# Performance work log

Hardware: AMD Instinct MI355X
Metric: run time of the kernel (lower is better)

Reference implementation:

```python
import jax, jax.numpy as jnp
import numpy as np

DIM, HEADS, DH, M, PINV_ITERS, RES_K = 512, 8, 64, 256, 6, 33

def layernorm(x, w, b, eps=1e-5):
    mu = jnp.mean(x, -1, keepdims=True)
    var = jnp.var(x, -1, keepdims=True)
    return (x - mu) * jax.lax.rsqrt(var + eps) * w + b

def pinv_iter(x, iters=PINV_ITERS):
    # Moore-Penrose iterative pseudo-inverse (lucidrains nystrom-attention)
    ax = jnp.abs(x)
    z = jnp.swapaxes(x, -1, -2) / (jnp.max(ax.sum(-1)) * jnp.max(ax.sum(-2)))
    I = jnp.eye(x.shape[-1], dtype=x.dtype)
    for _ in range(iters):
        xz = x @ z
        z = 0.25 * z @ (13 * I - xz @ (15 * I - xz @ (7 * I - xz)))
    return z

def _core(x, w_qkv):
    b, n, _ = x.shape
    pad = (M - n % M) % M            # Nystrom pads at the FRONT to a multiple of m=256
    xp = jnp.pad(x, ((0, 0), (pad, 0), (0, 0)))
    npad = n + pad
    q, k, v = jnp.split(xp @ w_qkv, 3, axis=-1)
    split_heads = lambda t: t.reshape(b, npad, HEADS, DH).transpose(0, 2, 1, 3)
    q = split_heads(q) * (DH ** -0.5)
    k, v = split_heads(k), split_heads(v)
    l = npad // M                    # tokens per landmark
    q_l = q.reshape(b, HEADS, M, l, DH).mean(3)
    k_l = k.reshape(b, HEADS, M, l, DH).mean(3)
    return q, k, v, q_l, k_l, pad, n

def nystrom_out(x, w_qkv, w_out, b_out, res_kernel):
    q, k, v, q_l, k_l, pad, n = _core(x, w_qkv)
    attn1 = jax.nn.softmax(jnp.einsum('bhid,bhjd->bhij', q, k_l), -1)    # (b,h,N,M)
    attn2 = jax.nn.softmax(jnp.einsum('bhid,bhjd->bhij', q_l, k_l), -1)  # (b,h,M,M)
    attn3 = jax.nn.softmax(jnp.einsum('bhid,bhjd->bhij', q_l, k), -1)    # (b,h,M,N)
    out = (attn1 @ pinv_iter(attn2)) @ (attn3 @ v)
    # depthwise residual conv over sequence dim, per head
    out = out + jax.lax.conv_general_dilated(
        v, res_kernel, (1, 1), [(RES_K // 2, RES_K // 2), (0, 0)],
        dimension_numbers=('NCHW', 'OIHW', 'NCHW'), feature_group_count=HEADS)
    b = out.shape[0]
    out = out.transpose(0, 2, 1, 3).reshape(b, -1, HEADS * DH) @ w_out + b_out
    return out[:, -n:]

def nystrom_cls_row(x, w_qkv):
    # cls-token (query index pad, head 0) row of attn1 @ pinv(attn2) @ attn3;
    # identical math to the full (n x n) matrix row the torch code slices out.
    q, k, v, q_l, k_l, pad, n = _core(x, w_qkv)
    q0, k0, ql0, kl0 = q[:, 0], k[:, 0], q_l[:, 0], k_l[:, 0]
    attn2 = jax.nn.softmax(ql0 @ jnp.swapaxes(kl0, -1, -2), -1)   # (b,M,M)
    attn3 = jax.nn.softmax(ql0 @ jnp.swapaxes(k0, -1, -2), -1)    # (b,M,N)
    row1 = jax.nn.softmax(jnp.einsum('bd,bjd->bj', q0[:, pad], kl0), -1)
    row = jnp.einsum('bj,bjk->bk', row1, pinv_iter(attn2))
    row = jnp.einsum('bk,bkn->bn', row, attn3)                    # (b, N_padded)
    return row, pad

def dwconv(x, k, b, p):
    y = jax.lax.conv_general_dilated(x, k, (1, 1), [(p, p), (p, p)],
        dimension_numbers=('NCHW', 'OIHW', 'NCHW'), feature_group_count=x.shape[1])
    return y + b[None, :, None, None]

def leff(x, k7, b7, k5, b5, k3, b3, Hs, Ws):
    cls_t, feat = x[:, :1], x[:, 1:]
    B, N, C = feat.shape
    img = feat.transpose(0, 2, 1).reshape(B, C, Hs, Ws)
    y = dwconv(img, k7, b7, 3) + img + dwconv(img, k5, b5, 2) + dwconv(img, k3, b3, 1)
    y = y.reshape(B, C, Hs * Ws).transpose(0, 2, 1)
    return jnp.concatenate([cls_t, y], axis=1)

def setup_inputs():
    key = jax.random.key(0)
    ks = iter(jax.random.split(key, 32))
    n, n_classes = 22500, 2
    p = {}
    p['h'] = jax.random.normal(next(ks), (n, 1024), jnp.float32)
    p['fc1_w'] = jax.random.normal(next(ks), (1024, DIM), jnp.float32) * 0.02
    p['fc1_b'] = jnp.zeros((DIM,), jnp.float32)
    p['cls_token'] = jax.random.normal(next(ks), (1, 1, DIM), jnp.float32)
    for pre in ('l1', 'l2'):
        p[pre + '_ln_w'] = jnp.ones((DIM,), jnp.float32)
        p[pre + '_ln_b'] = jnp.zeros((DIM,), jnp.float32)
        p[pre + '_wqkv'] = jax.random.normal(next(ks), (DIM, 3 * HEADS * DH), jnp.float32) * 0.02
        p[pre + '_wout'] = jax.random.normal(next(ks), (HEADS * DH, DIM), jnp.float32) * 0.02
        p[pre + '_bout'] = jnp.zeros((DIM,), jnp.float32)
        p[pre + '_resk'] = jax.random.normal(next(ks), (HEADS, 1, RES_K, 1), jnp.float32) * 0.05
    for kk in (7, 5, 3):
        p['leff_k%d' % kk] = jax.random.normal(next(ks), (DIM, 1, kk, kk), jnp.float32) * 0.05
        p['leff_b%d' % kk] = jnp.zeros((DIM,), jnp.float32)
    p['norm_w'] = jnp.ones((DIM,), jnp.float32)
    p['norm_b'] = jnp.zeros((DIM,), jnp.float32)
    p['fc2_w'] = jax.random.normal(next(ks), (DIM, n_classes), jnp.float32) * 0.02
    p['fc2_b'] = jnp.zeros((n_classes,), jnp.float32)
    return p

def reference(h, fc1_w, fc1_b, cls_token,
              l1_ln_w, l1_ln_b, l1_wqkv, l1_wout, l1_bout, l1_resk,
              leff_k7, leff_b7, leff_k5, leff_b5, leff_k3, leff_b3,
              l2_ln_w, l2_ln_b, l2_wqkv, l2_wout, l2_bout, l2_resk,
              norm_w, norm_b, fc2_w, fc2_b):
    x = h[None]                                   # (1, n, 1024)
    n = x.shape[1]
    x = jax.nn.relu(x @ fc1_w + fc1_b)            # (1, n, 512)
    Hs = int(np.ceil(np.sqrt(n)))                 # 150 for n=22500
    add_len = Hs * Hs - n
    if add_len > 0:
        x = jnp.concatenate([x, x[:, :add_len]], axis=1)
    x = jnp.concatenate([jnp.broadcast_to(cls_token, (1, 1, DIM)), x], axis=1)
    # TransLayer 1
    x = x + nystrom_out(layernorm(x, l1_ln_w, l1_ln_b), l1_wqkv, l1_wout, l1_bout, l1_resk)
    # LeFF positional layer
    x = leff(x, leff_k7, leff_b7, leff_k5, leff_b5, leff_k3, leff_b3, Hs, Hs)
    # TransLayer 2 (first call in TransMIL.forward)
    h2 = x + nystrom_out(layernorm(x, l2_ln_w, l2_ln_b), l2_wqkv, l2_wout, l2_bout, l2_resk)
    # TransLayer 2 second call: residual update then attention matrix of updated state
    h3 = h2 + nystrom_out(layernorm(h2, l2_ln_w, l2_ln_b), l2_wqkv, l2_wout, l2_bout, l2_resk)
    row, pad = nystrom_cls_row(layernorm(h3, l2_ln_w, l2_ln_b), l2_wqkv)
    A = row[0, pad + 1: pad + 1 + n][:, None]     # (n, 1) cls->instance attention
    hf = layernorm(h2, norm_w, norm_b)[:, 0]      # (1, 512)
    logits = hf @ fc2_w + fc2_b                   # (1, n_classes)
    Y_prob = jax.nn.softmax(logits, -1)
    return logits, Y_prob, A
```

## Files before the change

kernel.cpp:

```cpp
#include <hip/hip_runtime.h>

#define NTOK 22500
#define N1   22501
#define NPAD 22528
#define PADR 27
#define DIM  512
#define NH   8
#define DHD  64
#define MM   256
#define LLM  88
#define HSZ  150
#define CSZ  256
#define NCH  88

typedef short bf16x8 __attribute__((ext_vector_type(8)));
typedef float f32x4  __attribute__((ext_vector_type(4)));
typedef unsigned short us;

union U8 { bf16x8 v; unsigned short u[8]; };

__device__ __forceinline__ unsigned short f2b(float f){
  unsigned int u = __float_as_uint(f);
  unsigned int r = u + 0x7fffu + ((u>>16)&1u);
  return (unsigned short)(r>>16);
}
__device__ __forceinline__ float bf2f(unsigned short u){
  return __uint_as_float(((unsigned int)u)<<16);
}
__device__ __forceinline__ bf16x8 cvt8(float4 a, float4 b){
  U8 u;
  u.u[0]=f2b(a.x); u.u[1]=f2b(a.y); u.u[2]=f2b(a.z); u.u[3]=f2b(a.w);
  u.u[4]=f2b(b.x); u.u[5]=f2b(b.y); u.u[6]=f2b(b.z); u.u[7]=f2b(b.w);
  return u.v;
}
__device__ __forceinline__ void gld16(const void* g, void* l){
  __builtin_amdgcn_global_load_lds(
      (const __attribute__((address_space(1))) void*)g,
      (__attribute__((address_space(3))) void*)l, 16, 0, 0);
}

__device__ __forceinline__ float waveSum(float v){
#pragma unroll
  for (int o=32;o>0;o>>=1) v += __shfl_down(v,o);
  return v;
}
__device__ __forceinline__ float waveMax(float v){
#pragma unroll
  for (int o=32;o>0;o>>=1) v = fmaxf(v,__shfl_down(v,o));
  return v;
}
__device__ __forceinline__ float blockSum256(float v, float* sb){
  v = waveSum(v);
  __syncthreads();
  if ((threadIdx.x&63)==0) sb[threadIdx.x>>6]=v;
  __syncthreads();
  return sb[0]+sb[1]+sb[2]+sb[3];
}
__device__ __forceinline__ float blockMax256(float v, float* sb){
  v = waveMax(v);
  __syncthreads();
  if ((threadIdx.x&63)==0) sb[threadIdx.x>>6]=v;
  __syncthreads();
  return fmaxf(fmaxf(sb[0],sb[1]),fmaxf(sb[2],sb[3]));
}

__global__ void k_wT(const float* __restrict__ W, us* __restrict__ Bt, int K, int N)
{
  __shared__ float tile[32][33];
  int tx = threadIdx.x&31, ty = threadIdx.x>>5;
  int k0 = blockIdx.x*32, n0 = blockIdx.y*32;
#pragma unroll
  for (int i=0;i<4;++i){
    int k = k0+ty+i*8;
    if (k<K && n0+tx<N) tile[ty+i*8][tx] = W[(size_t)k*N + n0+tx];
  }
  __syncthreads();
#pragma unroll
  for (int i=0;i<4;++i){
    int n = n0+ty+i*8, k = k0+tx;
    if (n<N && k<K) Bt[(size_t)n*K + k] = f2b(tile[tx][ty+i*8]);
  }
}

__global__ void k_vT(const us* __restrict__ V, us* __restrict__ Vt)
{
  __shared__ us tile[32][33];
  int tx = threadIdx.x&31, ty = threadIdx.x>>5;
  int p0 = blockIdx.x*32;
  int h = blockIdx.y>>1, d0 = (blockIdx.y&1)*32;
#pragma unroll
  for (int i=0;i<4;++i){
    int p = p0+ty+i*8;
    tile[ty+i*8][tx] = V[((size_t)h*NPAD+p)*DHD + d0+tx];
  }
  __syncthreads();
#pragma unroll
  for (int i=0;i<4;++i){
    int d = d0+ty+i*8;
    Vt[((size_t)h*DHD+d)*NPAD + p0+tx] = tile[tx][ty+i*8];
  }
}

template<int MODE, int BM>
__global__ __launch_bounds__(256) void k_gemm(const float* __restrict__ Af,
    const us* __restrict__ Ab, const us* __restrict__ Bt, const float* __restrict__ bias,
    us* __restrict__ Xb, float* __restrict__ Cf, float* __restrict__ C2,
    us* __restrict__ Q_, us* __restrict__ K_, us* __restrict__ V_,
    const us* __restrict__ zpg, int Kd, int mtn)
{
  constexpr int ABUF = BM*64;
  __shared__ us SM[2*ABUF + 16384];
  const int tid = threadIdx.x;
  const int bid = blockIdx.x;
  const int ntile = bid / mtn;
  const int m0 = (bid % mtn)*BM, n0 = ntile*128;
  const int lane = tid & 63;
  const int wid = tid >> 6;
  constexpr int MT = BM/32;
  constexpr int ACH = BM/32;
  const int wm = (wid>>1)*(BM/2), wn = (wid&1)*64;
  f32x4 acc[MT][4] = {};
  const int NT = Kd >> 6;

  auto stage = [&](int t, int buf){
    us* As = SM + buf*ABUF;
    us* Bs = SM + 2*ABUF + buf*8192;
    int k0 = t*64;
    if (MODE==0){
#pragma unroll
      for (int i=0;i<BM/16;++i){
        int g = i*256 + tid;
        int row = g>>4, k4 = (g&15)*4;
        int gm = m0 + row;
        ushort4 h4 = make_ushort4(0,0,0,0);
        if (gm < NTOK){
          float4 v = *(const float4*)(Af + (size_t)gm*Kd + k0 + k4);
          h4.x=f2b(v.x); h4.y=f2b(v.y); h4.z=f2b(v.z); h4.w=f2b(v.w);
        }
        *(ushort4*)(&As[row*64 + (k4 ^ ((row&7)<<3))]) = h4;
      }
    } else {
#pragma unroll
      for (int i=0;i<ACH;++i){
        int c = wid*ACH+i;
        int row = c*8 + (lane>>3);
        int scol8 = ((lane&7) ^ (row&7))*8;
        int gm = m0+row;
        const us* ga;
        if (MODE==2) ga = Ab + ((size_t)((gm<N1?gm:0)+PADR))*Kd + k0 + scol8;
        else ga = (gm>=PADR) ? Ab + (size_t)(gm-PADR)*Kd + k0 + scol8 : zpg + scol8;
        gld16(ga, &As[c*512]);
      }
    }
#pragma unroll
    for (int i=0;i<4;++i){
      int c = wid*4+i;
      int row = c*8 + (lane>>3);
      int scol8 = ((lane&7) ^ (row&7))*8;
      int vn = n0+row;
      if (MODE==3) vn = (vn<64)? vn : vn+448;
      gld16(Bt + (size_t)vn*Kd + k0 + scol8, &Bs[c*512]);
    }
  };

  stage(0, 0);
  __syncthreads();
  for (int t=0; t<NT; ++t){
    const int cur = t&1;
    if (t+1 < NT) stage(t+1, cur^1);
    us* As = SM + cur*ABUF;
    us* Bs = SM + 2*ABUF + cur*8192;
#pragma unroll
    for (int ks=0; ks<2; ++ks){
      const int kk = ks*32 + (lane>>4)*8;
      bf16x8 af[MT], bfm[4];
#pragma unroll
      for (int tt=0;tt<MT;++tt){
        int r = wm + tt*16 + (lane&15);
        af[tt] = *(bf16x8*)(&As[r*64 + (kk ^ ((r&7)<<3))]);
      }
#pragma unroll
      for (int tt=0;tt<4;++tt){
        int c = wn + tt*16 + (lane&15);
        bfm[tt] = *(bf16x8*)(&Bs[c*64 + (kk ^ ((c&7)<<3))]);
      }
#pragma unroll
      for (int mt=0;mt<MT;++mt)
#pragma unroll
        for (int nt=0;nt<4;++nt)
          acc[mt][nt] = __builtin_amdgcn_mfma_f32_16x16x32_bf16(af[mt], bfm[nt], acc[mt][nt], 0,0,0);
    }
    __syncthreads();
  }
  const int rbase = (lane>>4)*4;
  const int cl = lane&15;
  if (MODE==3){
#pragma unroll
    for (int mt=0;mt<MT;++mt)
#pragma unroll
      for (int r=0;r<4;++r){
        int gm = m0 + wm + mt*16 + rbase + r;
#pragma unroll
        for (int nt=0;nt<4;++nt){
          int gn = n0 + wn + nt*16 + cl;
          float v = acc[mt][nt][r];
          if (gn < 64) Cf[(size_t)gm*DHD + gn] = v*0.125f;
          else         C2[(size_t)gm*DHD + (gn-64)] = v;
        }
      }
    return;
  }
  const float sc1 = (MODE==1 && (ntile>>2)==0) ? 0.125f : 1.f;
#pragma unroll
  for (int mt=0;mt<MT;++mt)
#pragma unroll
    for (int r=0;r<4;++r){
      int row = wm + mt*16 + rbase + r;
#pragma unroll
      for (int nt=0;nt<4;++nt){
        int col = wn + nt*16 + cl;
        float v = acc[mt][nt][r];
        if (MODE==0){ v += bias[n0+col]; v = v>0.f?v:0.f; }
        else if (MODE==2){ v += bias[n0+col]; }
        else v *= sc1;
        SM[row*128 + col] = f2b(v);
      }
    }
  __syncthreads();
  if (MODE==1){
    const int sec = ntile>>2;
    us* dst = sec==0 ? Q_ : (sec==1 ? K_ : V_);
#pragma unroll
    for (int i=0;i<BM/16;++i){
      int v8 = i*256 + tid;
      int row = v8>>4, c8 = (v8&15)*8;
      int gm = m0 + row, gn = n0 + c8;
      int hh = (gn>>6)&7, d = gn&63;
      *(bf16x8*)(dst + ((size_t)hh*NPAD+gm)*DHD + d) = *(bf16x8*)(&SM[row*128 + c8]);
    }
  } else if (MODE==0){
#pragma unroll
    for (int i=0;i<BM/16;++i){
      int v8 = i*256 + tid;
      int row = v8>>4, c8 = (v8&15)*8;
      int gm = m0 + row;
      if (gm < NTOK)
        *(bf16x8*)(Xb + (size_t)(1+gm)*DIM + n0 + c8) = *(bf16x8*)(&SM[row*128 + c8]);
    }
  } else {
#pragma unroll
    for (int i=0;i<BM/16;++i){
      int v8 = i*256 + tid;
      int row = v8>>4, c8 = (v8&15)*8;
      int gm = m0 + row;
      if (gm < N1){
        us* p = Xb + (size_t)gm*DIM + n0 + c8;
        U8 xo, ad, o;
        xo.v = *(bf16x8*)p;
        ad.v = *(bf16x8*)(&SM[row*128 + c8]);
#pragma unroll
        for (int j=0;j<8;++j) o.u[j] = f2b(bf2f(xo.u[j]) + bf2f(ad.u[j]));
        *(bf16x8*)p = o.v;
      }
    }
  }
}

__global__ void k_setcls(us* __restrict__ X, const float* __restrict__ cls){
  int i = blockIdx.x*256 + threadIdx.x;
  if (i < DIM) X[i] = f2b(cls[i]);
}
__global__ void k_copyu(us* __restrict__ d, const us* __restrict__ s, size_t n){
  size_t i = (size_t)blockIdx.x*256 + threadIdx.x;
  if (i<n) d[i]=s[i];
}

__global__ void k_ln(const us* __restrict__ X, us* __restrict__ Y,
                     const float* __restrict__ w, const float* __restrict__ b)
{
  __shared__ float sb[4];
  const us* x = X + (size_t)blockIdx.x*DIM;
  us* y = Y + (size_t)blockIdx.x*DIM;
  int t = threadIdx.x;
  ushort2 xv = *(const ushort2*)(x + 2*t);
  float a0=bf2f(xv.x), a1=bf2f(xv.y);
  float s = blockSum256(a0+a1, sb);
  float q = blockSum256(a0*a0+a1*a1, sb);
  float mean = s*(1.f/512.f);
  float var = q*(1.f/512.f) - mean*mean;
  float rstd = rsqrtf(var+1e-5f);
  float2 wv = *(const float2*)(w + 2*t);
  float2 bv = *(const float2*)(b + 2*t);
  ushort2 o;
  o.x = f2b((a0-mean)*rstd*wv.x+bv.x);
  o.y = f2b((a1-mean)*rstd*wv.y+bv.y);
  *(ushort2*)(y + 2*t) = o;
}

__global__ void k_landmark2(const us* __restrict__ Q, const us* __restrict__ K,
                            us* __restrict__ QL, us* __restrict__ KL)
{
  int hm = blockIdx.x;
  bool isK = hm >= NH*MM;
  if (isK) hm -= NH*MM;
  int h = hm>>8, m = hm&255; int d = threadIdx.x;
  const us* base = (isK?K:Q) + ((size_t)h*NPAD + (size_t)m*LLM)*DHD + d;
  float s = 0.f;
  for (int j=0;j<LLM;++j) s += bf2f(base[(size_t)j*DHD]);
  (isK?KL:QL)[((size_t)h*MM + m)*DHD + d] = f2b(s * (1.f/(float)LLM));
}
__global__ void k_landmark2f(const float* __restrict__ Q, const float* __restrict__ K,
                             float* __restrict__ QL, float* __restrict__ KL)
{
  int hm = blockIdx.x;
  bool isK = hm >= MM;
  int m = isK ? hm-MM : hm; int d = threadIdx.x;
  const float* base = (isK?K:Q) + (size_t)m*LLM*DHD + d;
  float s = 0.f;
  for (int j=0;j<LLM;++j) s += base[(size_t)j*DHD];
  (isK?KL:QL)[(size_t)m*DHD + d] = s * (1.f/(float)LLM);
}

__global__ __launch_bounds__(64) void k_nt64(const float* __restrict__ A,
    const float* __restrict__ B, float* __restrict__ C,
    long sA, long sB, long sC, int Nr)
{
  int lane = threadIdx.x;
  int n0 = blockIdx.x*64, m0 = blockIdx.y*64;
  A += (size_t)blockIdx.z*sA; B += (size_t)blockIdx.z*sB; C += (size_t)blockIdx.z*sC;
  f32x4 acc[4][4] = {};
#pragma unroll
  for (int ks=0;ks<2;++ks){
    int kk = ks*32 + (lane>>4)*8;
    bf16x8 af[4], bfr[4];
#pragma unroll
    for (int mt=0;mt<4;++mt){
      const float* p = A + (size_t)(m0+mt*16+(lane&15))*64 + kk;
      af[mt] = cvt8(*(const float4*)p, *(const float4*)(p+4));
    }
#pragma unroll
    for (int nt=0;nt<4;++nt){
      const float* p = B + (size_t)(n0+nt*16+(lane&15))*64 + kk;
      bfr[nt] = cvt8(*(const float4*)p, *(const float4*)(p+4));
    }
#pragma unroll
    for (int mt=0;mt<4;++mt)
#pragma unroll
      for (int nt=0;nt<4;++nt)
        acc[mt][nt] = __builtin_amdgcn_mfma_f32_16x16x32_bf16(af[mt], bfr[nt], acc[mt][nt], 0,0,0);
  }
#pragma unroll
  for (int mt=0;mt<4;++mt)
#pragma unroll
    for (int r=0;r<4;++r){
      int row = m0+mt*16+(lane>>4)*4+r;
#pragma unroll
      for (int nt=0;nt<4;++nt){
        int col = n0+nt*16+(lane&15);
        C[(size_t)row*Nr + col] = acc[mt][nt][r];
      }
    }
}

__global__ __launch_bounds__(64) void k_nt64b(const us* __restrict__ A,
    const us* __restrict__ B, float* __restrict__ C,
    long sA, long sB, long sC, int Nr)
{
  int lane = threadIdx.x;
  int n0 = blockIdx.x*64, m0 = blockIdx.y*64;
  A += (size_t)blockIdx.z*sA; B += (size_t)blockIdx.z*sB; C += (size_t)blockIdx.z*sC;
  f32x4 acc[4][4] = {};
#pragma unroll
  for (int ks=0;ks<2;++ks){
    int kk = ks*32 + (lane>>4)*8;
    bf16x8 af[4], bfr[4];
#pragma unroll
    for (int mt=0;mt<4;++mt)
      af[mt] = *(const bf16x8*)(A + (size_t)(m0+mt*16+(lane&15))*64 + kk);
#pragma unroll
    for (int nt=0;nt<4;++nt)
      bfr[nt] = *(const bf16x8*)(B + (size_t)(n0+nt*16+(lane&15))*64 + kk);
#pragma unroll
    for (int mt=0;mt<4;++mt)
#pragma unroll
      for (int nt=0;nt<4;++nt)
        acc[mt][nt] = __builtin_amdgcn_mfma_f32_16x16x32_bf16(af[mt], bfr[nt], acc[mt][nt], 0,0,0);
  }
#pragma unroll
  for (int mt=0;mt<4;++mt)
#pragma unroll
    for (int r=0;r<4;++r){
      int row = m0+mt*16+(lane>>4)*4+r;
#pragma unroll
      for (int nt=0;nt<4;++nt){
        int col = n0+nt*16+(lane&15);
        C[(size_t)row*Nr + col] = acc[mt][nt][r];
      }
    }
}

template<int PM>
__global__ __launch_bounds__(256) void k_pgemm(const us* __restrict__ A,
    const us* __restrict__ Bt, us* __restrict__ C, us* __restrict__ Ct,
    float dc, float alpha, int writeC)
{
  __shared__ us As[64*256];
  __shared__ us Bs[64*256];
  const int tid = threadIdx.x, lane = tid&63, wid = tid>>6;
  const int n0 = blockIdx.x*64, m0 = blockIdx.y*64;
  const us* Ab = A + (size_t)blockIdx.z*65536;
  const us* Bb = Bt + (size_t)blockIdx.z*65536;
  for (int i=tid; i<4096; i+=256){
    int r = i>>6, c4 = (i&63)*4;
    *(ushort4*)(&As[r*256 + (c4 ^ ((r&7)<<3))]) = *(const ushort4*)(Ab + (size_t)(m0+r)*256 + c4);
    *(ushort4*)(&Bs[r*256 + (c4 ^ ((r&7)<<3))]) = *(const ushort4*)(Bb + (size_t)(n0+r)*256 + c4);
  }
  __syncthreads();
  const int wm = (wid>>1)*32, wn = (wid&1)*32;
  f32x4 acc[2][2] = {};
#pragma unroll
  for (int ks=0;ks<8;++ks){
    int kk = ks*32 + (lane>>4)*8;
    bf16x8 af[2], bfr[2];
#pragma unroll
    for (int t=0;t<2;++t){
      int rr = wm + t*16 + (lane&15);
      af[t] = *(const bf16x8*)(&As[rr*256 + (kk ^ ((rr&7)<<3))]);
      int cc = wn + t*16 + (lane&15);
      bfr[t] = *(const bf16x8*)(&Bs[cc*256 + (kk ^ ((cc&7)<<3))]);
    }
#pragma unroll
    for (int mt=0;mt<2;++mt)
#pragma unroll
      for (int nt=0;nt<2;++nt)
        acc[mt][nt] = __builtin_amdgcn_mfma_f32_16x16x32_bf16(af[mt], bfr[nt], acc[mt][nt], 0,0,0);
  }
  float vv[2][4][2];
#pragma unroll
  for (int mt=0;mt<2;++mt)
#pragma unroll
    for (int q=0;q<4;++q){
      int rl = wm + mt*16 + (lane>>4)*4 + q;
#pragma unroll
      for (int nt=0;nt<2;++nt){
        int clx = wn + nt*16 + (lane&15);
        float v = acc[mt][nt][q];
        if (PM==1) v = alpha*(dc*bf2f(As[rl*256 + (clx ^ ((rl&7)<<3))]) - v);
        vv[mt][q][nt] = v;
      }
    }
  __syncthreads();
  us* TT = As;
#pragma unroll
  for (int mt=0;mt<2;++mt)
#pragma unroll
    for (int q=0;q<4;++q){
      int rl = wm + mt*16 + (lane>>4)*4 + q;
      int sw = (rl&7)<<3;
#pragma unroll
      for (int nt=0;nt<2;++nt){
        int clx = wn + nt*16 + (lane&15);
        TT[rl*64 + (clx ^ sw)] = f2b(vv[mt][q][nt]);
      }
    }
  __syncthreads();
  {
    int c = tid>>2, r0 = (tid&3)*16;
    U8 b0, b1;
#pragma unroll
    for (int i=0;i<8;++i){
      int r = r0+i;       b0.u[i] = TT[r*64 + (c ^ ((r&7)<<3))];
      int r2 = r0+8+i;    b1.u[i] = TT[r2*64 + (c ^ ((r2&7)<<3))];
    }
    us* dst = Ct + (size_t)blockIdx.z*65536 + (size_t)(n0+c)*256 + m0 + r0;
    *(bf16x8*)dst = b0.v;
    *(bf16x8*)(dst+8) = b1.v;
  }
  if (PM==0 || writeC){
    int rr = tid>>2, c0 = (tid&3)*16;
    int sw = (rr&7)<<3;
    bf16x8 x0 = *(const bf16x8*)(&TT[rr*64 + (c0 ^ sw)]);
    bf16x8 x1 = *(const bf16x8*)(&TT[rr*64 + ((c0+8) ^ sw)]);
    us* dc2 = C + (size_t)blockIdx.z*65536 + (size_t)(m0+rr)*256 + n0 + c0;
    *(bf16x8*)dc2 = x0;
    *(bf16x8*)(dc2+8) = x1;
  }
}

__global__ __launch_bounds__(256) void k_pgemm2(const us* __restrict__ A,
    const us* __restrict__ Bt, us* __restrict__ Ct)
{
  __shared__ us As[16384];
  __shared__ us Bs[16384];
  const int tid = threadIdx.x, lane = tid&63, wid = tid>>6;
  const int n0 = 0, m0 = blockIdx.y*64;
  const us* Ab = A + (size_t)blockIdx.z*65536;
  const us* Bb = Bt + (size_t)blockIdx.z*16384;
  for (int i=tid; i<4096; i+=256){
    int r = i>>6, c4 = (i&63)*4;
    *(ushort4*)(&As[r*256 + (c4 ^ ((r&7)<<3))]) = *(const ushort4*)(Ab + (size_t)(m0+r)*256 + c4);
    if (r < 64)
      *(ushort4*)(&Bs[r*256 + (c4 ^ ((r&7)<<3))]) = *(const ushort4*)(Bb + (size_t)(n0+r)*256 + c4);
  }
  __syncthreads();
  const int wm = (wid>>1)*32, wn = (wid&1)*32;
  f32x4 acc[2][2] = {};
#pragma unroll
  for (int ks=0;ks<8;++ks){
    int kk = ks*32 + (lane>>4)*8;
    bf16x8 af[2], bfr[2];
#pragma unroll
    for (int t=0;t<2;++t){
      int rr = wm + t*16 + (lane&15);
      af[t] = *(const bf16x8*)(&As[rr*256 + (kk ^ ((rr&7)<<3))]);
      int cc = wn + t*16 + (lane&15);
      bfr[t] = *(const bf16x8*)(&Bs[cc*256 + (kk ^ ((cc&7)<<3))]);
    }
#pragma unroll
    for (int mt=0;mt<2;++mt)
#pragma unroll
      for (int nt=0;nt<2;++nt)
        acc[mt][nt] = __builtin_amdgcn_mfma_f32_16x16x32_bf16(af[mt], bfr[nt], acc[mt][nt], 0,0,0);
  }
#pragma unroll
  for (int mt=0;mt<2;++mt)
#pragma unroll
    for (int r=0;r<4;++r){
      int row = m0 + wm + mt*16 + (lane>>4)*4 + r;
#pragma unroll
      for (int nt=0;nt<2;++nt){
        int col = n0 + wn + nt*16 + (lane&15);
        Ct[(size_t)blockIdx.z*16384 + (size_t)col*256 + row] = f2b(acc[mt][nt][r]);
      }
    }
}

__global__ void k_softmax256(float* __restrict__ S, us* __restrict__ Sb)
{
  __shared__ float sb[4];
  float* row = S + ((size_t)blockIdx.x<<8);
  float x = row[threadIdx.x];
  float m = blockMax256(x, sb);
  float e = __expf(x-m);
  float s = blockSum256(e, sb);
  float p = e/s;
  row[threadIdx.x] = p;
  Sb[((size_t)blockIdx.x<<8) + threadIdx.x] = f2b(p);
}
__global__ void k_csmax(const float* __restrict__ A2, float* __restrict__ sums)
{
  __shared__ float sb[4];
  int b = blockIdx.x, j = threadIdx.x;
  const float* Ab = A2 + ((size_t)b<<16);
  float s = 0.f;
// ... 170 lines not shown
}

__global__ __launch_bounds__(256) void k_attn1(const us* __restrict__ Qb,
    const us* __restrict__ KLb, const us* __restrict__ WmT,
    us* __restrict__ OH)
{
  __shared__ us KWs[64*256];
  __shared__ us Ps[64*256];
  int h = blockIdx.y, tid = threadIdx.x;
  int wid = tid>>6, lane = tid&63;
  int q0 = blockIdx.x*64;
  for (int i=tid; i<4096; i+=256){
    int lm = i>>4, k4 = (i&15)*4;
    *(ushort4*)(&KWs[lm*64 + (k4 ^ ((lm&7)<<3))]) =
        *(const ushort4*)(KLb + ((size_t)h*MM + lm)*DHD + k4);
  }
  bf16x8 aq[2];
  const us* qp = Qb + ((size_t)h*NPAD + q0 + wid*16 + (lane&15))*DHD;
#pragma unroll
  for (int ks=0;ks<2;++ks)
    aq[ks] = *(const bf16x8*)(qp + ks*32 + (lane>>4)*8);
  __syncthreads();
  f32x4 s[16];
#pragma unroll
  for (int nt=0;nt<16;++nt) s[nt] = (f32x4){0.f,0.f,0.f,0.f};
#pragma unroll
  for (int ks=0;ks<2;++ks){
    int kk = ks*32 + (lane>>4)*8;
#pragma unroll
    for (int nt=0;nt<16;++nt){
      int col = nt*16 + (lane&15);
      bf16x8 b = *(const bf16x8*)(&KWs[col*64 + (kk ^ ((col&7)<<3))]);
      s[nt] = __builtin_amdgcn_mfma_f32_16x16x32_bf16(aq[ks], b, s[nt], 0,0,0);
    }
  }
  float rcp[4];
#pragma unroll
  for (int r=0;r<4;++r){
    float m = -1e30f;
#pragma unroll
    for (int nt=0;nt<16;++nt) m = fmaxf(m, s[nt][r]);
#pragma unroll
    for (int off=8;off>=1;off>>=1) m = fmaxf(m, __shfl_xor(m, off));
    float l = 0.f;
#pragma unroll
    for (int nt=0;nt<16;++nt){ float p=__expf(s[nt][r]-m); s[nt][r]=p; l+=p; }
#pragma unroll
    for (int off=8;off>=1;off>>=1) l += __shfl_xor(l, off);
    rcp[r] = 1.f/l;
  }
  int prow_base = wid*16 + (lane>>4)*4;
#pragma unroll
  for (int nt=0;nt<16;++nt){
    int col = nt*16 + (lane&15);
#pragma unroll
    for (int r=0;r<4;++r){
      int row = prow_base + r;
      Ps[row*256 + (col ^ ((row&7)<<3))] = f2b(s[nt][r]);
    }
  }
  __syncthreads();
  for (int i=tid; i<4096; i+=256){
    int d = i>>6, k4 = (i&63)*4;
    ushort4 u = *(const ushort4*)(WmT + ((size_t)h*DHD + d)*MM + k4);
    *(ushort4*)(&KWs[d*256 + (k4 ^ ((d&7)<<3))]) = u;
  }
  __syncthreads();
  f32x4 acc[4] = {};
  int arow = wid*16 + (lane&15);
#pragma unroll
  for (int ks=0;ks<8;++ks){
    int kk = ks*32 + (lane>>4)*8;
    bf16x8 a = *(const bf16x8*)(&Ps[arow*256 + (kk ^ ((arow&7)<<3))]);
#pragma unroll
    for (int dt=0;dt<4;++dt){
      int d = dt*16 + (lane&15);
      bf16x8 b = *(const bf16x8*)(&KWs[d*256 + (kk ^ ((d&7)<<3))]);
      acc[dt] = __builtin_amdgcn_mfma_f32_16x16x32_bf16(a, b, acc[dt], 0,0,0);
    }
  }
#pragma unroll
  for (int r=0;r<4;++r){
    int row = q0 + prow_base + r;
    us* op = OH + (size_t)row*DIM + h*DHD;
#pragma unroll
    for (int dt=0;dt<4;++dt)
      op[dt*16 + (lane&15)] = f2b(acc[dt][r]*rcp[r]);
  }
}

#define SCBLK 32
__global__ __launch_bounds__(256) void k_seqconv(const us* __restrict__ Vb,
    const float* __restrict__ resk, us* __restrict__ OH)
{
  __shared__ us Vs[64*512];
  int tid = threadIdx.x;
  int p0 = blockIdx.x*SCBLK;
  for (int i=tid; i<16384; i+=256){
    int pl = i>>8, c2 = i&255;
    int gp = p0 - 16 + pl;
    int hh = c2>>5, d2 = (c2&31)*2;
    ushort2 v = make_ushort2(0,0);
    if (gp>=0 && gp<NPAD) v = *(const ushort2*)(Vb + ((size_t)hh*NPAD+gp)*DHD + d2);
    *(ushort2*)(&Vs[pl*512 + c2*2]) = v;
  }
  __syncthreads();
  int h = tid>>5;
  float kr[33];
#pragma unroll
  for (int r=0;r<33;++r) kr[r] = resk[h*33+r];
  for (int pl=0; pl<SCBLK; ++pl){
    float s0=0.f, s1=0.f;
#pragma unroll
    for (int r=0;r<33;++r){
      ushort2 v = *(const ushort2*)(&Vs[(pl+r)*512 + tid*2]);
      s0 += bf2f(v.x)*kr[r];
      s1 += bf2f(v.y)*kr[r];
    }
    size_t o = (size_t)(p0+pl)*DIM + tid*2;
    ushort2 cur = *(ushort2*)(OH + o);
    *(ushort2*)(OH + o) = make_ushort2(f2b(bf2f(cur.x)+s0), f2b(bf2f(cur.y)+s1));
  }
}

__global__ void k_tfwd(const us* __restrict__ X, us* __restrict__ T)
{
  __shared__ us tile[32][33];
  int tx = threadIdx.x & 31, ty = threadIdx.x >> 5;
  int s0 = blockIdx.x*32, c0 = blockIdx.y*32;
  for (int yy=0; yy<4; ++yy){
    int s = s0 + ty + yy*8;
    if (s < NTOK) tile[ty+yy*8][tx] = X[(size_t)(1+s)*DIM + c0+tx];
  }
  __syncthreads();
  for (int yy=0; yy<4; ++yy){
    int c = c0 + ty + yy*8;
    int s = s0 + tx;
    if (s < NTOK) T[(size_t)c*NTOK + s] = tile[tx][ty+yy*8];
  }
}
__global__ void k_tbwd(const us* __restrict__ T, us* __restrict__ X)
{
  __shared__ us tile[32][33];
  int tx = threadIdx.x & 31, ty = threadIdx.x >> 5;
  int s0 = blockIdx.x*32, c0 = blockIdx.y*32;
  for (int yy=0; yy<4; ++yy){
    int c = c0 + ty + yy*8, s = s0 + tx;
    if (s < NTOK) tile[ty+yy*8][tx] = T[(size_t)c*NTOK + s];
  }
  __syncthreads();
  for (int yy=0; yy<4; ++yy){
    int s = s0 + ty + yy*8, c = c0 + tx;
    if (s < NTOK) X[(size_t)(1+s)*DIM + c] = tile[tx][ty+yy*8];
  }
}
__global__ __launch_bounds__(256) void k_leff(const us* __restrict__ T,
    const float* __restrict__ k7, const float* __restrict__ b7,
    const float* __restrict__ k5, const float* __restrict__ b5,
    const float* __restrict__ k3, const float* __restrict__ b3,
    us* __restrict__ T2)
{
  __shared__ float tile[21*21];
  int c = blockIdx.y;
  int ti = blockIdx.x/10, tj = blockIdx.x%10;
  int i0 = ti*15-3, j0 = tj*15-3;
  const us* img = T + (size_t)c*NTOK;
  for (int idx=threadIdx.x; idx<441; idx+=256){
    int ii = idx/21, jj = idx%21;
    int gi = i0+ii, gj = j0+jj;
    tile[idx] = (gi>=0 && gi<HSZ && gj>=0 && gj<HSZ) ? bf2f(img[gi*HSZ+gj]) : 0.f;
  }
  __syncthreads();
  if (threadIdx.x < 225){
    int li = threadIdx.x/15, lj = threadIdx.x%15;
    int gi = ti*15+li, gj = tj*15+lj;
    float acc = tile[(li+3)*21 + (lj+3)] + b7[c]+b5[c]+b3[c];
    const float* w7 = k7 + c*49;
#pragma unroll
    for (int a=0;a<7;++a)
#pragma unroll
      for (int bb=0;bb<7;++bb) acc += tile[(li+a)*21 + (lj+bb)]*w7[a*7+bb];
    const float* w5 = k5 + c*25;
#pragma unroll
    for (int a=0;a<5;++a)
#pragma unroll
      for (int bb=0;bb<5;++bb) acc += tile[(li+1+a)*21 + (lj+1+bb)]*w5[a*5+bb];
    const float* w3 = k3 + c*9;
#pragma unroll
    for (int a=0;a<3;++a)
#pragma unroll
      for (int bb=0;bb<3;++bb) acc += tile[(li+2+a)*21 + (lj+2+bb)]*w3[a*3+bb];
    T2[(size_t)c*NTOK + gi*HSZ+gj] = f2b(acc);
  }
}

__global__ void k_row1(const float* __restrict__ Q0, const float* __restrict__ KL0,
                       float* __restrict__ row1)
{
  __shared__ float sb[4];
  __shared__ float qv[64];
  int t = threadIdx.x;
  if (t<64) qv[t] = Q0[PADR*DHD + t];
  __syncthreads();
  float l = 0.f;
#pragma unroll
  for (int d=0;d<64;++d) l += qv[d]*KL0[(size_t)t*DHD+d];
  float m = blockMax256(l, sb);
  float e = __expf(l-m);
  float s = blockSum256(e, sb);
  row1[t] = e/s;
}
__global__ void k_rz(const float* __restrict__ row1, const us* __restrict__ Zt,
                     float* __restrict__ rz)
{
  __shared__ float r1[256];
  int t = threadIdx.x;
  r1[t] = row1[t];
  __syncthreads();
  float s = 0.f;
  for (int k2=0;k2<256;++k2) s += r1[k2]*bf2f(Zt[(size_t)t*MM + k2]);
  rz[t] = s;
}
__global__ void k_rowstat(const float* __restrict__ L0, float* __restrict__ mx, float* __restrict__ se)
{
  __shared__ float sb[4];
  const float* row = L0 + (size_t)blockIdx.x*NPAD;
  float m = -1e30f;
  for (int i=threadIdx.x;i<NPAD;i+=256) m = fmaxf(m, row[i]);
  m = blockMax256(m, sb);
  float s = 0.f;
  for (int i=threadIdx.x;i<NPAD;i+=256) s += __expf(row[i]-m);
  s = blockSum256(s, sb);
  if (threadIdx.x==0){ mx[blockIdx.x]=m; se[blockIdx.x]=s; }
}
__global__ void k_aout(const float* __restrict__ L0, const float* __restrict__ rz,
    const float* __restrict__ mx, const float* __restrict__ se, float* __restrict__ out)
{
  __shared__ float wk[256], mk[256];
  int t = threadIdx.x;
  wk[t] = rz[t]/se[t];
  mk[t] = mx[t];
  __syncthreads();
  int p = blockIdx.x*256 + t;
  if (p >= NTOK) return;
  size_t pp = (size_t)(PADR+1+p);
  float a = 0.f;
  for (int k2=0;k2<256;++k2) a += wk[k2]*__expf(L0[(size_t)k2*NPAD+pp]-mk[k2]);
  out[4+p] = a;
}
__global__ void k_final(const us* __restrict__ H2r, const float* __restrict__ nw,
    const float* __restrict__ nbb, const float* __restrict__ w2, const float* __restrict__ b2,
    float* __restrict__ out)
{
  __shared__ float sb[4];
  __shared__ float hf[512];
  int t = threadIdx.x;
  float x0 = bf2f(H2r[t]), x1 = bf2f(H2r[256+t]);
  float s = blockSum256(x0+x1, sb);
  float q = blockSum256(x0*x0+x1*x1, sb);
  float mean = s*(1.f/512.f);
  float var = q*(1.f/512.f) - mean*mean;
  float rstd = rsqrtf(var+1e-5f);
  hf[t]     = (x0-mean)*rstd*nw[t]+nbb[t];
  hf[256+t] = (x1-mean)*rstd*nw[256+t]+nbb[256+t];
  __syncthreads();
  float p0 = hf[t]*w2[t*2]   + hf[256+t]*w2[(256+t)*2];
  float p1 = hf[t]*w2[t*2+1] + hf[256+t]*w2[(256+t)*2+1];
  p0 = blockSum256(p0, sb);
  p1 = blockSum256(p1, sb);
  if (t==0){
    float l0 = p0+b2[0], l1 = p1+b2[1];
    float m = fmaxf(l0,l1);
    float e0 = __expf(l0-m), e1 = __expf(l1-m), si = 1.f/(e0+e1);
    out[0]=l0; out[1]=l1; out[2]=e0*si; out[3]=e1*si;
  }
}

struct Bufs {
  float *A2,*sums,*scl,*Pmax,*Psum;
  us *Xb,*Yb,*OHb,*Qb,*Kb,*Vb,*Vtb,*QLb,*KLb,*A2b;
  us *Z0b,*Z0tb,*Z1b,*Z1tb,*XZb,*XZtb,*T1tb,*T2tb;
  us *A3Vtb,*WmT,*Pacc,*zpg;
};

static void run_pinv(const us* A2b, Bufs& b, int NB, hipStream_t st)
{
  dim3 g(4,4,NB);
  us *Zc=b.Z0b, *Zct=b.Z0tb, *Zn=b.Z1b, *Znt=b.Z1tb;
  for (int it=0; it<6; ++it){
    k_pgemm<0><<<g,256,0,st>>>(A2b, Zct, b.XZb, b.XZtb, 0.f, 1.f, 1);
    k_pgemm<1><<<g,256,0,st>>>(b.XZb, b.XZtb, nullptr, b.T1tb, 7.f, 1.f, 0);
    k_pgemm<1><<<g,256,0,st>>>(b.XZb, b.T1tb, nullptr, b.T2tb, 15.f, 1.f, 0);
    k_pgemm<1><<<g,256,0,st>>>(Zc, b.T2tb, Zn, Znt, 13.f, 0.25f, 1);
    us* t1=Zc; Zc=Zn; Zn=t1;
    us* t2=Zct; Zct=Znt; Znt=t2;
  }
}

static void nystrom_layer(Bufs& b, const float* lnw, const float* lnb,
    const us* wqkvT, const us* woutT,
    const float* bout, const float* resk, hipStream_t st)
{
  k_ln<<<N1,256,0,st>>>(b.Xb, b.Yb, lnw, lnb);
  k_gemm<1,128><<<176*12,256,0,st>>>(nullptr, b.Yb, wqkvT, nullptr,
      nullptr, nullptr, nullptr, b.Qb, b.Kb, b.Vb, b.zpg, DIM, 176);
  k_vT<<<dim3(NPAD/32,16),256,0,st>>>(b.Vb, b.Vtb);
  k_landmark2<<<2*NH*MM,64,0,st>>>(b.Qb, b.Kb, b.QLb, b.KLb);
  k_nt64b<<<dim3(4,4,NH),64,0,st>>>(b.QLb, b.KLb, b.A2,
      (long)MM*DHD,(long)MM*DHD,(long)MM*MM, MM);
  k_softmax256<<<NH*MM,256,0,st>>>(b.A2, b.A2b);
  k_csmax<<<NH,256,0,st>>>(b.A2, b.sums);
  k_scale2<<<1,256,0,st>>>(b.sums, b.scl, NH);
  k_z0t<<<dim3(8,8*NH),256,0,st>>>(b.A2, b.Z0b, b.Z0tb, b.scl);
  run_pinv(b.A2b, b, NH, st);
  k_attn3<<<dim3(NCH,NH),256,0,st>>>(b.QLb, b.Kb, b.Vtb, b.Pmax, b.Psum, b.Pacc);
  k_attn3_merge<<<NH*MM,64,0,st>>>(b.Pmax, b.Psum, b.Pacc, b.A3Vtb);
  k_pgemm2<<<dim3(1,4,NH),256,0,st>>>(b.Z0b, b.A3Vtb, b.WmT);
  k_attn1<<<dim3(NPAD/64,NH),256,0,st>>>(b.Qb, b.KLb, b.WmT, b.OHb);
  k_seqconv<<<NPAD/SCBLK,256,0,st>>>(b.Vb, resk, b.OHb);
  k_gemm<2,64><<<352*4,256,0,st>>>(nullptr, b.OHb, woutT, bout,
      b.Xb, nullptr, nullptr, nullptr, nullptr, nullptr, b.zpg, DIM, 352);
}

extern "C" void kernel_launch(void* const* d_in, const int* in_sizes, int n_in,
                              void* d_out, int out_size, void* d_ws, size_t ws_size,
                              hipStream_t stream)
{
  (void)n_in; (void)out_size;
  bool sig_order = (in_sizes[10] == 25088);
  int iL2 = sig_order ? 16 : 10;
  int iLf = sig_order ? 10 : 16;

  const float* h       = (const float*)d_in[0];
  const float* fc1_w   = (const float*)d_in[1];
  const float* fc1_b   = (const float*)d_in[2];
  const float* cls_tok = (const float*)d_in[3];
  const float* l1_lnw  = (const float*)d_in[4];
  const float* l1_lnb  = (const float*)d_in[5];
  const float* l1_wqkv = (const float*)d_in[6];
  const float* l1_wout = (const float*)d_in[7];
  const float* l1_bout = (const float*)d_in[8];
  const float* l1_resk = (const float*)d_in[9];
  const float* l2_lnw  = (const float*)d_in[iL2+0];
  const float* l2_lnb  = (const float*)d_in[iL2+1];
  const float* l2_wqkv = (const float*)d_in[iL2+2];
  const float* l2_wout = (const float*)d_in[iL2+3];
  const float* l2_bout = (const float*)d_in[iL2+4];
  const float* l2_resk = (const float*)d_in[iL2+5];
  const float* k7 = (const float*)d_in[iLf+0];
  const float* b7 = (const float*)d_in[iLf+1];
  const float* k5 = (const float*)d_in[iLf+2];
  const float* b5 = (const float*)d_in[iLf+3];
  const float* k3 = (const float*)d_in[iLf+4];
  const float* b3 = (const float*)d_in[iLf+5];
  const float* nw = (const float*)d_in[22];
  const float* nbb= (const float*)d_in[23];
  const float* w2 = (const float*)d_in[24];
  const float* b2 = (const float*)d_in[25];
  float* out = (float*)d_out;

  char* base = (char*)d_ws;
  auto allocF = [&](size_t n)->float*{
    float* p=(float*)base; base += ((n*sizeof(float)+255)&~(size_t)255); return p; };
  auto allocU = [&](size_t n)->us*{
    us* p=(us*)base; base += ((n*sizeof(us)+255)&~(size_t)255); return p; };

  const size_t S = (size_t)NPAD*DIM;
  const size_t SQ = (size_t)MM*MM;
  Bufs b;
  b.Xb  = allocU(S);
  b.Yb  = allocU(S);
  b.OHb = allocU(S);
  b.Qb  = allocU(S);
  b.Kb  = allocU(S);
  b.Vb  = allocU(S);
  b.Vtb = allocU(S);
  b.QLb = allocU((size_t)NH*MM*DHD);
  b.KLb = allocU((size_t)NH*MM*DHD);
  b.A2  = allocF((size_t)NH*SQ);
  b.A2b = allocU((size_t)NH*SQ);
  b.Z0b = allocU((size_t)NH*SQ);  b.Z0tb = allocU((size_t)NH*SQ);
  b.Z1b = allocU((size_t)NH*SQ);  b.Z1tb = allocU((size_t)NH*SQ);
  b.XZb = allocU((size_t)NH*SQ);  b.XZtb = allocU((size_t)NH*SQ);
  b.T1tb= allocU((size_t)NH*SQ);
  b.T2tb= allocU((size_t)NH*SQ);
  b.A3Vtb = allocU((size_t)NH*MM*DHD);
  b.WmT   = allocU((size_t)NH*MM*DHD);
  b.sums  = allocF(2*(size_t)NH*MM);
  b.scl   = allocF(16);
  b.Pmax  = allocF((size_t)NH*NCH*MM);
  b.Psum  = allocF((size_t)NH*NCH*MM);
  b.Pacc  = allocU((size_t)NH*NCH*MM*DHD);
  b.zpg   = allocU(512);
  us* fc1T   = allocU((size_t)DIM*1024);
  us* wqkvT1 = allocU((size_t)1536*DIM);
  us* wqkvT2 = allocU((size_t)1536*DIM);
  us* woutT1 = allocU((size_t)DIM*DIM);
  us* woutT2 = allocU((size_t)DIM*DIM);
  float* Q0   = allocF((size_t)NPAD*DHD);
  float* K0   = allocF((size_t)NPAD*DHD);
  float* QL0f = allocF((size_t)MM*DHD);
  float* KL0f = allocF((size_t)MM*DHD);
  float* row1 = allocF(256);
  float* rzv  = allocF(256);
  float* mxv  = allocF(256);
  float* sev  = allocF(256);
  us* h2row = allocU(512);
  if ((size_t)(base - (char*)d_ws) > ws_size) return;

  hipMemsetAsync((void*)b.zpg, 0, 1024, stream);

  k_wT<<<dim3(32,16),256,0,stream>>>(fc1_w, fc1T, 1024, DIM);
  k_wT<<<dim3(16,48),256,0,stream>>>(l1_wqkv, wqkvT1, DIM, 1536);
  k_wT<<<dim3(16,48),256,0,stream>>>(l2_wqkv, wqkvT2, DIM, 1536);
  k_wT<<<dim3(16,16),256,0,stream>>>(l1_wout, woutT1, DIM, DIM);
  k_wT<<<dim3(16,16),256,0,stream>>>(l2_wout, woutT2, DIM, DIM);

  k_gemm<0,64><<<352*4,256,0,stream>>>(h, nullptr, fc1T, fc1_b,
      b.Xb, nullptr, nullptr, nullptr, nullptr, nullptr, b.zpg, 1024, 352);
  k_setcls<<<2,256,0,stream>>>(b.Xb, cls_tok);

  nystrom_layer(b, l1_lnw, l1_lnb, wqkvT1, woutT1, l1_bout, l1_resk, stream);
  k_tfwd<<<dim3(704,16),256,0,stream>>>(b.Xb, b.OHb);
  k_leff<<<dim3(100,512),256,0,stream>>>(b.OHb, k7,b7,k5,b5,k3,b3, b.Qb);
  k_tbwd<<<dim3(704,16),256,0,stream>>>(b.Qb, b.Xb);

  nystrom_layer(b, l2_lnw, l2_lnb, wqkvT2, woutT2, l2_bout, l2_resk, stream);
  k_copyu<<<2,256,0,stream>>>(h2row, b.Xb, 512);

  nystrom_layer(b, l2_lnw, l2_lnb, wqkvT2, woutT2, l2_bout, l2_resk, stream);

  k_ln<<<N1,256,0,stream>>>(b.Xb, b.Yb, l2_lnw, l2_lnb);
  k_gemm<3,64><<<352,256,0,stream>>>(nullptr, b.Yb, wqkvT2, nullptr,
      nullptr, Q0, K0, nullptr, nullptr, nullptr, b.zpg, DIM, 352);
  k_landmark2f<<<2*MM,64,0,stream>>>(Q0, K0, QL0f, KL0f);
  k_nt64<<<dim3(4,4,1),64,0,stream>>>(QL0f, KL0f, b.A2, 0,0,0, MM);
  k_softmax256<<<MM,256,0,stream>>>(b.A2, b.A2b);
  k_csmax<<<1,256,0,stream>>>(b.A2, b.sums);
  k_scale2<<<1,256,0,stream>>>(b.sums, b.scl, 1);
  k_z0t<<<dim3(8,8),256,0,stream>>>(b.A2, b.Z0b, b.Z0tb, b.scl);
  run_pinv(b.A2b, b, 1, stream);
  k_row1<<<1,256,0,stream>>>(Q0, KL0f, row1);
  k_rz<<<1,256,0,stream>>>(row1, b.Z0tb, rzv);
  float* L0 = (float*)b.Yb;
  k_nt64<<<dim3(NPAD/64,4,1),64,0,stream>>>(QL0f, K0, L0, 0,0,0, NPAD);
  k_rowstat<<<MM,256,0,stream>>>(L0, mxv, sev);
  k_aout<<<88,256,0,stream>>>(L0, rzv, mxv, sev, out);
  k_final<<<1,256,0,stream>>>(h2row, nw, nbb, w2, b2, out);
}
```

Measured before the change: 2.380 ms.

## Triple-buffer GEMM loads with async prefetch and pre-convert fc1 input to bf16

New measurement: 2.370 ms. No clear change (-0.4%).

```diff
diff --git a/kernel.cpp b/kernel.cpp
--- a/kernel.cpp
+++ b/kernel.cpp
@@ -64,6 +64,16 @@
   return fmaxf(fmaxf(sb[0],sb[1]),fmaxf(sb[2],sb[3]));
 }
 
+__global__ void k_cvt(const float* __restrict__ src, us* __restrict__ dst, size_t n4)
+{
+  size_t i = ((size_t)blockIdx.x*256 + threadIdx.x);
+  if (i < n4){
+    float4 v = *(const float4*)(src + i*4);
+    ushort4 u; u.x=f2b(v.x); u.y=f2b(v.y); u.z=f2b(v.z); u.w=f2b(v.w);
+    *(ushort4*)(dst + i*4) = u;
+  }
+}
+
 __global__ void k_wT(const float* __restrict__ W, us* __restrict__ Bt, int K, int N)
 {
   __shared__ float tile[32][33];
@@ -101,56 +111,41 @@
   }
 }
 
-template<int MODE, int BM>
-__global__ __launch_bounds__(256) void k_gemm(const float* __restrict__ Af,
+template<int MODE>
+__global__ __launch_bounds__(256) void k_gemm(
     const us* __restrict__ Ab, const us* __restrict__ Bt, const float* __restrict__ bias,
     us* __restrict__ Xb, float* __restrict__ Cf, float* __restrict__ C2,
     us* __restrict__ Q_, us* __restrict__ K_, us* __restrict__ V_,
     const us* __restrict__ zpg, int Kd, int mtn)
 {
-  constexpr int ABUF = BM*64;
-  __shared__ us SM[2*ABUF + 16384];
+  constexpr int BM = 64;
+  constexpr int BUFE = BM*64 + 128*64;
+  __shared__ us SM[3*BUFE];
   const int tid = threadIdx.x;
   const int bid = blockIdx.x;
   const int ntile = bid / mtn;
   const int m0 = (bid % mtn)*BM, n0 = ntile*128;
   const int lane = tid & 63;
   const int wid = tid >> 6;
-  constexpr int MT = BM/32;
-  constexpr int ACH = BM/32;
-  const int wm = (wid>>1)*(BM/2), wn = (wid&1)*64;
-  f32x4 acc[MT][4] = {};
+  const int wm = (wid>>1)*32, wn = (wid&1)*64;
+  f32x4 acc[2][4] = {};
   const int NT = Kd >> 6;
 
   auto stage = [&](int t, int buf){
-    us* As = SM + buf*ABUF;
-    us* Bs = SM + 2*ABUF + buf*8192;
+    us* As = SM + buf*BUFE;
+    us* Bs = As + BM*64;
     int k0 = t*64;
-    if (MODE==0){
-#pragma unroll
-      for (int i=0;i<BM/16;++i){
-        int g = i*256 + tid;
-        int row = g>>4, k4 = (g&15)*4;
-        int gm = m0 + row;
-        ushort4 h4 = make_ushort4(0,0,0,0);
-        if (gm < NTOK){
-          float4 v = *(const float4*)(Af + (size_t)gm*Kd + k0 + k4);
-          h4.x=f2b(v.x); h4.y=f2b(v.y); h4.z=f2b(v.z); h4.w=f2b(v.w);
-        }
-        *(ushort4*)(&As[row*64 + (k4 ^ ((row&7)<<3))]) = h4;
-      }
-    } else {
-#pragma unroll
-      for (int i=0;i<ACH;++i){
-        int c = wid*ACH+i;
-        int row = c*8 + (lane>>3);
-        int scol8 = ((lane&7) ^ (row&7))*8;
-        int gm = m0+row;
-        const us* ga;
-        if (MODE==2) ga = Ab + ((size_t)((gm<N1?gm:0)+PADR))*Kd + k0 + scol8;
-        else ga = (gm>=PADR) ? Ab + (size_t)(gm-PADR)*Kd + k0 + scol8 : zpg + scol8;
-        gld16(ga, &As[c*512]);
-      }
+#pragma unroll
+    for (int i=0;i<2;++i){
+      int c = wid*2+i;
+      int row = c*8 + (lane>>3);
+      int scol8 = ((lane&7) ^ (row&7))*8;
+      int gm = m0+row;
+      const us* ga;
+      if (MODE==0)      ga = (gm<NTOK) ? Ab + (size_t)gm*Kd + k0 + scol8 : zpg + scol8;
+      else if (MODE==2) ga = Ab + ((size_t)((gm<N1?gm:0)+PADR))*Kd + k0 + scol8;
+      else              ga = (gm>=PADR) ? Ab + (size_t)(gm-PADR)*Kd + k0 + scol8 : zpg + scol8;
+      gld16(ga, &As[c*512]);
     }
 #pragma unroll
     for (int i=0;i<4;++i){
@@ -164,18 +159,20 @@
   };
 
   stage(0, 0);
-  __syncthreads();
+  stage(1, 1);
   for (int t=0; t<NT; ++t){
-    const int cur = t&1;
-    if (t+1 < NT) stage(t+1, cur^1);
-    us* As = SM + cur*ABUF;
-    us* Bs = SM + 2*ABUF + cur*8192;
+    asm volatile("s_waitcnt vmcnt(6)" ::: "memory");
+    __builtin_amdgcn_s_barrier();
+    asm volatile("" ::: "memory");
+    if (t+2 < NT) stage(t+2, (t+2)%3);
+    us* As = SM + (t%3)*BUFE;
+    us* Bs = As + BM*64;
 #pragma unroll
     for (int ks=0; ks<2; ++ks){
       const int kk = ks*32 + (lane>>4)*8;
-      bf16x8 af[MT], bfm[4];
-#pragma unroll
-      for (int tt=0;tt<MT;++tt){
+      bf16x8 af[2], bfm[4];
+#pragma unroll
+      for (int tt=0;tt<2;++tt){
         int r = wm + tt*16 + (lane&15);
         af[tt] = *(bf16x8*)(&As[r*64 + (kk ^ ((r&7)<<3))]);
       }
@@ -185,18 +182,18 @@
         bfm[tt] = *(bf16x8*)(&Bs[c*64 + (kk ^ ((c&7)<<3))]);
       }
 #pragma unroll
-      for (int mt=0;mt<MT;++mt)
+      for (int mt=0;mt<2;++mt)
 #pragma unroll
         for (int nt=0;nt<4;++nt)
           acc[mt][nt] = __builtin_amdgcn_mfma_f32_16x16x32_bf16(af[mt], bfm[nt], acc[mt][nt], 0,0,0);
     }
-    __syncthreads();
-  }
+  }
+  __syncthreads();
   const int rbase = (lane>>4)*4;
   const int cl = lane&15;
   if (MODE==3){
 #pragma unroll
-    for (int mt=0;mt<MT;++mt)
+    for (int mt=0;mt<2;++mt)
 #pragma unroll
       for (int r=0;r<4;++r){
         int gm = m0 + wm + mt*16 + rbase + r;
@@ -212,7 +209,7 @@
   }
   const float sc1 = (MODE==1 && (ntile>>2)==0) ? 0.125f : 1.f;
 #pragma unroll
-  for (int mt=0;mt<MT;++mt)
+  for (int mt=0;mt<2;++mt)
 #pragma unroll
     for (int r=0;r<4;++r){
       int row = wm + mt*16 + rbase + r;
@@ -231,7 +228,7 @@
     const int sec = ntile>>2;
     us* dst = sec==0 ? Q_ : (sec==1 ? K_ : V_);
 #pragma unroll
-    for (int i=0;i<BM/16;++i){
+    for (int i=0;i<4;++i){
       int v8 = i*256 + tid;
       int row = v8>>4, c8 = (v8&15)*8;
       int gm = m0 + row, gn = n0 + c8;
@@ -240,7 +237,7 @@
     }
   } else if (MODE==0){
 #pragma unroll
-    for (int i=0;i<BM/16;++i){
+    for (int i=0;i<4;++i){
       int v8 = i*256 + tid;
       int row = v8>>4, c8 = (v8&15)*8;
       int gm = m0 + row;
@@ -249,7 +246,7 @@
     }
   } else {
 #pragma unroll
-    for (int i=0;i<BM/16;++i){
+    for (int i=0;i<4;++i){
       int v8 = i*256 + tid;
       int row = v8>>4, c8 = (v8&15)*8;
       int gm = m0 + row;
@@ -1026,8 +1023,8 @@
     const float* bout, const float* resk, hipStream_t st)
 {
   k_ln<<<N1,256,0,st>>>(b.Xb, b.Yb, lnw, lnb);
-  k_gemm<1,128><<<176*12,256,0,st>>>(nullptr, b.Yb, wqkvT, nullptr,
-      nullptr, nullptr, nullptr, b.Qb, b.Kb, b.Vb, b.zpg, DIM, 176);
+  k_gemm<1><<<352*12,256,0,st>>>(b.Yb, wqkvT, nullptr,
+      nullptr, nullptr, nullptr, b.Qb, b.Kb, b.Vb, b.zpg, DIM, 352);
   k_vT<<<dim3(NPAD/32,16),256,0,st>>>(b.Vb, b.Vtb);
   k_landmark2<<<2*NH*MM,64,0,st>>>(b.Qb, b.Kb, b.QLb, b.KLb);
   k_nt64b<<<dim3(4,4,NH),64,0,st>>>(b.QLb, b.KLb, b.A2,
@@ -1042,7 +1039,7 @@
   k_pgemm2<<<dim3(1,4,NH),256,0,st>>>(b.Z0b, b.A3Vtb, b.WmT);
   k_attn1<<<dim3(NPAD/64,NH),256,0,st>>>(b.Qb, b.KLb, b.WmT, b.OHb);
   k_seqconv<<<NPAD/SCBLK,256,0,st>>>(b.Vb, resk, b.OHb);
-  k_gemm<2,64><<<352*4,256,0,st>>>(nullptr, b.OHb, woutT, bout,
+  k_gemm<2><<<352*4,256,0,st>>>(b.OHb, woutT, bout,
       b.Xb, nullptr, nullptr, nullptr, nullptr, nullptr, b.zpg, DIM, 352);
 }
 
@@ -1116,6 +1113,7 @@
   b.Psum  = allocF((size_t)NH*NCH*MM);
   b.Pacc  = allocU((size_t)NH*NCH*MM*DHD);
   b.zpg   = allocU(512);
+  us* hb     = allocU((size_t)NTOK*1024);
   us* fc1T   = allocU((size_t)DIM*1024);
   us* wqkvT1 = allocU((size_t)1536*DIM);
   us* wqkvT2 = allocU((size_t)1536*DIM);
@@ -1134,13 +1132,14 @@
 
   hipMemsetAsync((void*)b.zpg, 0, 1024, stream);
 
+  k_cvt<<<((size_t)NTOK*1024/4 + 255)/256,256,0,stream>>>(h, hb, (size_t)NTOK*1024/4);
   k_wT<<<dim3(32,16),256,0,stream>>>(fc1_w, fc1T, 1024, DIM);
   k_wT<<<dim3(16,48),256,0,stream>>>(l1_wqkv, wqkvT1, DIM, 1536);
   k_wT<<<dim3(16,48),256,0,stream>>>(l2_wqkv, wqkvT2, DIM, 1536);
   k_wT<<<dim3(16,16),256,0,stream>>>(l1_wout, woutT1, DIM, DIM);
   k_wT<<<dim3(16,16),256,0,stream>>>(l2_wout, woutT2, DIM, DIM);
 
-  k_gemm<0,64><<<352*4,256,0,stream>>>(h, nullptr, fc1T, fc1_b,
+  k_gemm<0><<<352*4,256,0,stream>>>(hb, fc1T, fc1_b,
       b.Xb, nullptr, nullptr, nullptr, nullptr, nullptr, b.zpg, 1024, 352);
   k_setcls<<<2,256,0,stream>>>(b.Xb, cls_tok);
 
@@ -1155,7 +1154,7 @@
   nystrom_layer(b, l2_lnw, l2_lnb, wqkvT2, woutT2, l2_bout, l2_resk, stream);
 
   k_ln<<<N1,256,0,stream>>>(b.Xb, b.Yb, l2_lnw, l2_lnb);
-  k_gemm<3,64><<<352,256,0,stream>>>(nullptr, b.Yb, wqkvT2, nullptr,
+  k_gemm<3><<<352,256,0,stream>>>(b.Yb, wqkvT2, nullptr,
       nullptr, Q0, K0, nullptr, nullptr, nullptr, b.zpg, DIM, 352);
   k_landmark2f<<<2*MM,64,0,stream>>>(Q0, K0, QL0f, KL0f);
   k_nt64<<<dim3(4,4,1),64,0,stream>>>(QL0f, KL0f, b.A2, 0,0,0, MM);
```
